# Kernel optimization log

Hardware: AMD Instinct MI355X
Metric: run time of the kernel (lower is better)

## Reference

```python
import jax, jax.numpy as jnp
import numpy as np

B, T, H, D = 1, 4096, 8, 64
CHUNK = 1024
SCALE = 0.125  # 1/sqrt(head_size)
EPS = 1e-6


def setup_inputs() -> dict:
    key = jax.random.key(0)
    k1, k2, k3, k4 = jax.random.split(key, 4)
    q = jax.random.normal(k1, (B, T, H, D), jnp.float32)
    k = jax.random.normal(k2, (B, T, H, D), jnp.float32)
    v = jax.random.normal(k3, (B, T, H, D), jnp.float32)
    # log gates: small negative values (log of per-token decay in (0,1])
    log_g = -0.05 * jax.random.uniform(k4, (B, T, H), jnp.float32)
    return {"q": q, "k": k, "v": v, "log_g": log_g}


def _power_retention(q, k, v, log_g):
    """Chunked degree-2 power retention with log-gating.

    score(t,s) = exp(g_t - g_s) * (scale * q_t . k_s)^2  (causal),
    where g = cumsum(log_g). Cross-chunk part carried via expanded state
    S[h,d,e,v] = sum_s w_s k_d k_e v  (phi(k) = k (x) k, since (q.k)^2 = phi(q).phi(k))
    and sum-of-keys normalizer s[h,d,e]. out = num / max(den, eps).
    """
    Bq, Tq, Hq, Dq = q.shape
    C, L = Tq // CHUNK, CHUNK
    qs = (q * SCALE).reshape(Bq, C, L, Hq, Dq)   # fold scale into q
    kc = k.reshape(Bq, C, L, Hq, Dq)
    vc = v.reshape(Bq, C, L, Hq, Dq)
    g = jnp.cumsum(log_g.reshape(Bq, C, L, Hq), axis=2)  # [B,C,L,H] in-chunk cum gate
    g_end = g[:, :, -1, :]                                # [B,C,H]

    # ---- intra-chunk (parallel form) ----
    scores = jnp.einsum('bclhd,bcshd->bclsh', qs, kc)          # [B,C,L,S,H]
    logdec = g[:, :, :, None, :] - g[:, :, None, :, :]          # g_t - g_s
    causal = jnp.arange(L)[:, None] >= jnp.arange(L)[None, :]
    A = jnp.where(causal[None, None, :, :, None],
                  jnp.exp(logdec) * scores * scores, 0.0)       # [B,C,L,S,H]
    intra = jnp.einsum('bclsh,bcshv->bclhv', A, vc)             # [B,C,L,H,Dv]
    row = A.sum(axis=3)                                         # [B,C,L,H]

    # ---- per-chunk state contributions ----
    wk = jnp.exp(g_end[:, :, None, :] - g)                      # key-side decay to chunk end
    kw = kc * wk[..., None]
    P = jnp.einsum('bclhd,bclhe,bclhv->bchdev', kw, kc, vc)     # [B,C,H,D,D,Dv]
    Z = jnp.einsum('bclhd,bclhe->bchde', kw, kc)                # [B,C,H,D,D]
    qdec = jnp.exp(g)                                           # query-side decay from chunk start
    gtot = jnp.exp(g_end)                                       # whole-chunk decay

    def step(carry, xs):
        S, sk = carry
        qc, Pc, Zc, gd, gt = xs   # qc [B,L,H,D], Pc [B,H,D,D,Dv], gd [B,L,H], gt [B,H]
        inter = jnp.einsum('blhd,blhe,bhdev->blhv', qc, qc, S) * gd[..., None]
        den_i = jnp.einsum('blhd,blhe,bhde->blh', qc, qc, sk) * gd
        S = gt[:, :, None, None, None] * S + Pc
        sk = gt[:, :, None, None] * sk + Zc
        return (S, sk), (inter, den_i)

    S0 = jnp.zeros((Bq, Hq, Dq, Dq, Dq), q.dtype)
    sk0 = jnp.zeros((Bq, Hq, Dq, Dq), q.dtype)
    xs = (jnp.moveaxis(qs, 1, 0), jnp.moveaxis(P, 1, 0), jnp.moveaxis(Z, 1, 0),
          jnp.moveaxis(qdec, 1, 0), jnp.moveaxis(gtot, 1, 0))
    (_, _), (inter, den_i) = jax.lax.scan(step, (S0, sk0), xs)
    inter = jnp.moveaxis(inter, 0, 1)   # [B,C,L,H,Dv]
    den_i = jnp.moveaxis(den_i, 0, 1)   # [B,C,L,H]

    num = intra + inter
    den = jnp.maximum(row + den_i, EPS)
    out = num / den[..., None]
    return out.reshape(Bq, Tq, Hq, Dq)


def reference(q, k, v, log_g):
    return _power_retention(q, k, v, log_g)
```

## Files before the change

kernel.cpp:

```cpp
#include <hip/hip_runtime.h>
#include <math.h>

typedef float f32x4 __attribute__((ext_vector_type(4)));
typedef __bf16 bf16x8 __attribute__((ext_vector_type(8)));
typedef __bf16 bf16x4 __attribute__((ext_vector_type(4)));

namespace {
constexpr int NC = 4, CL = 1024, NH = 8, ND = 64;
constexpr float KSCALE = 0.125f, KEPS = 1e-6f;
constexpr int PQ = 72;
constexpr int PK = 40;
}

#define MFMA(a,b,c) __builtin_amdgcn_mfma_f32_16x16x32_bf16((a),(b),(c),0,0,0)

__global__ __launch_bounds__(1024) void gate_kernel(const float* __restrict__ lg,
    float* __restrict__ g_arr, float* __restrict__ gend, float* __restrict__ gtot) {
  int c = blockIdx.x >> 3, h = blockIdx.x & 7;
  int l = threadIdx.x;
  __shared__ float sm[CL];
  sm[l] = lg[(c*CL + l)*NH + h];
  __syncthreads();
  for (int off = 1; off < CL; off <<= 1) {
    float t = (l >= off) ? sm[l-off] : 0.f;
    __syncthreads();
    sm[l] += t;
    __syncthreads();
  }
  g_arr[(c*NH + h)*CL + l] = sm[l];
  if (l == 0) { gend[c*NH+h] = sm[CL-1]; gtot[c*NH+h] = expf(sm[CL-1]); }
}

__global__ __launch_bounds__(256) void convert_kernel(const float* __restrict__ q,
    const float* __restrict__ k, const float* __restrict__ v,
    const float* __restrict__ g_arr, const float* __restrict__ gend,
    __bf16* __restrict__ qgb, __bf16* __restrict__ kgb,
    __bf16* __restrict__ kht, __bf16* __restrict__ vt) {
  int lt = blockIdx.x, h = blockIdx.y, c = blockIdx.z;
  int ch = c*NH + h;
  int t = threadIdx.x;
  __shared__ float ld[64][65];
  int lr = t >> 2, sg = t & 3;
  int l = lt*64 + lr;
  size_t ib = ((size_t)(c*CL + l)*NH + h)*ND + sg*16;
  float ge = gend[ch];
  float gl = g_arr[ch*CL + l];
  float eq = expf(0.5f*gl), ekk = expf(-0.5f*gl), ew = expf(0.5f*(ge-gl));
  float qv[16], kv[16], vv[16];
  #pragma unroll
  for (int i = 0; i < 4; ++i) {
    *(f32x4*)&qv[4*i] = *(const f32x4*)&q[ib+4*i];
    *(f32x4*)&kv[4*i] = *(const f32x4*)&k[ib+4*i];
    *(f32x4*)&vv[4*i] = *(const f32x4*)&v[ib+4*i];
  }
  size_t ob = ((size_t)ch*CL + l)*ND + sg*16;
  {
    bf16x8 a, b;
    #pragma unroll
    for (int i = 0; i < 8; ++i) { a[i]=(__bf16)(qv[i]*KSCALE*eq); b[i]=(__bf16)(qv[8+i]*KSCALE*eq); }
    *(bf16x8*)&qgb[ob] = a; *(bf16x8*)&qgb[ob+8] = b;
    #pragma unroll
    for (int i = 0; i < 8; ++i) { a[i]=(__bf16)(kv[i]*ekk); b[i]=(__bf16)(kv[8+i]*ekk); }
    *(bf16x8*)&kgb[ob] = a; *(bf16x8*)&kgb[ob+8] = b;
  }
  #pragma unroll
  for (int i = 0; i < 16; ++i) ld[lr][sg*16+i] = kv[i]*ew;
  __syncthreads();
  {
    int d = t >> 2, s2 = t & 3;
    bf16x8 a, b;
    #pragma unroll
    for (int i = 0; i < 8; ++i) { a[i]=(__bf16)ld[s2*16+i][d]; b[i]=(__bf16)ld[s2*16+8+i][d]; }
    size_t kb = ((size_t)ch*ND + d)*CL + lt*64 + s2*16;
    *(bf16x8*)&kht[kb] = a; *(bf16x8*)&kht[kb+8] = b;
  }
  __syncthreads();
  #pragma unroll
  for (int i = 0; i < 16; ++i) ld[lr][sg*16+i] = vv[i];
  __syncthreads();
  {
    int p = t >> 2, s2 = t & 3;
    bf16x8 a, b;
    #pragma unroll
    for (int i = 0; i < 8; ++i) { a[i]=(__bf16)ld[s2*16+i][p]; b[i]=(__bf16)ld[s2*16+8+i][p]; }
    size_t vb = ((size_t)ch*80 + p)*CL + lt*64 + s2*16;
    *(bf16x8*)&vt[vb] = a; *(bf16x8*)&vt[vb+8] = b;
  }
  if (t < 64) vt[((size_t)ch*80 + 64)*CL + lt*64 + t] = (__bf16)1.0f;
  for (int idx = t; idx < 15*64; idx += 256)
    vt[((size_t)ch*80 + 65 + idx/64)*CL + lt*64 + (idx & 63)] = (__bf16)0.0f;
}

__global__ __launch_bounds__(256) void intra_kernel(const __bf16* __restrict__ qgb,
    const __bf16* __restrict__ kgb, const __bf16* __restrict__ vt,
    float* __restrict__ out, float* __restrict__ rowp) {
  int rt = blockIdx.x, h = blockIdx.y, c = blockIdx.z;
  int ch = c*NH + h;
  int t = threadIdx.x, wv = t >> 6, lane = t & 63, qq = lane >> 4, lm = lane & 15;
  __shared__ __align__(16) __bf16 qt[64*PQ];
  __shared__ __align__(16) __bf16 kgl[32*PQ];
  __shared__ __align__(16) __bf16 vtl[80*PK];
  __shared__ __align__(16) __bf16 As[64*PK];
  {
    int r = t >> 2, sg = t & 3;
    size_t gb = ((size_t)ch*CL + rt*64 + r)*ND + sg*16;
    *(bf16x8*)&qt[r*PQ + sg*16]     = *(const bf16x8*)&qgb[gb];
    *(bf16x8*)&qt[r*PQ + sg*16 + 8] = *(const bf16x8*)&qgb[gb+8];
  }
  __syncthreads();
  bf16x8 bq0 = *(bf16x8*)&qt[(wv*16+lm)*PQ + qq*8];
  bf16x8 bq1 = *(bf16x8*)&qt[(wv*16+lm)*PQ + 32 + qq*8];
  f32x4 acc[5];
  #pragma unroll
  for (int n = 0; n < 5; ++n) acc[n] = (f32x4){0.f,0.f,0.f,0.f};
  int r_gc = rt*64 + wv*16 + lm;
  int nst = 2*rt + 2;
  for (int s3 = 0; s3 < nst; ++s3) {
    __syncthreads();
    {
      int r = t >> 3, sg = t & 7;
      *(bf16x8*)&kgl[r*PQ + sg*8] =
        *(const bf16x8*)&kgb[((size_t)ch*CL + s3*32 + r)*ND + sg*8];
      int r2 = t >> 2, s2 = t & 3;
      *(bf16x8*)&vtl[r2*PK + s2*8] =
        *(const bf16x8*)&vt[((size_t)ch*80 + r2)*CL + s3*32 + s2*8];
      if (t < 64)
        *(bf16x8*)&vtl[(64+r2)*PK + s2*8] =
          *(const bf16x8*)&vt[((size_t)ch*80 + 64 + r2)*CL + s3*32 + s2*8];
    }
    __syncthreads();
    #pragma unroll
    for (int ss = 0; ss < 2; ++ss) {
      f32x4 dr = (f32x4){0.f,0.f,0.f,0.f};
      bf16x8 a0 = *(bf16x8*)&kgl[(ss*16+lm)*PQ + qq*8];
      bf16x8 a1 = *(bf16x8*)&kgl[(ss*16+lm)*PQ + 32 + qq*8];
      dr = MFMA(a0, bq0, dr);
      dr = MFMA(a1, bq1, dr);
      bf16x4 pk;
      #pragma unroll
      for (int j = 0; j < 4; ++j) {
        int s_g = s3*32 + ss*16 + qq*4 + j;
        float dv = dr[j];
        pk[j] = (__bf16)((s_g <= r_gc) ? dv*dv : 0.f);
      }
      *(bf16x4*)&As[(wv*16+lm)*PK + ss*16 + qq*4] = pk;
    }
    bf16x8 aav = *(bf16x8*)&As[(wv*16+lm)*PK + qq*8];
    #pragma unroll
    for (int n = 0; n < 5; ++n) {
      bf16x8 bv = *(bf16x8*)&vtl[(n*16+lm)*PK + qq*8];
      acc[n] = MFMA(aav, bv, acc[n]);
    }
  }
  if (c == 0) {
    #pragma unroll
    for (int j = 0; j < 4; ++j) {
      float rs = __shfl(acc[4][j], lane & 48, 64);
      float dinv = 1.f / fmaxf(rs, KEPS);
      int rg = rt*64 + wv*16 + qq*4 + j;
      size_t ob = ((size_t)(c*CL + rg)*NH + h)*ND + lm;
      #pragma unroll
      for (int n = 0; n < 4; ++n) out[ob + 16*n] = acc[n][j]*dinv;
    }
  } else {
    #pragma unroll
    for (int j = 0; j < 4; ++j) {
      int rg = rt*64 + wv*16 + qq*4 + j;
      size_t ob = ((size_t)(c*CL + rg)*NH + h)*ND + lm;
      #pragma unroll
      for (int n = 0; n < 4; ++n) out[ob + 16*n] = acc[n][j];
      if (lm == 0) rowp[ch*CL + rg] = acc[4][j];
    }
  }
}

__global__ __launch_bounds__(256) void pzscan_kernel(const __bf16* __restrict__ kht,
    const __bf16* __restrict__ vt, const float* __restrict__ gtot,
    __bf16* __restrict__ st) {
  int mblk = blockIdx.x, h = blockIdx.y;
  int t = threadIdx.x, wv = t >> 6, lane = t & 63, qq = lane >> 4, lm = lane & 15;
  __shared__ __align__(16) __bf16 ke[64*PK];
  __shared__ __align__(16) __bf16 kd[2*PK];
  __shared__ __align__(16) __bf16 vtl[80*PK];
  __shared__ float tb[64][72];
  int dl = wv >> 1, e0w = (wv & 1)*32;
  f32x4 S_reg[2][5];
  #pragma unroll
  for (int m = 0; m < 2; ++m)
    #pragma unroll
    for (int n = 0; n < 5; ++n) S_reg[m][n] = (f32x4){0.f,0.f,0.f,0.f};
  for (int cc = 0; cc < 3; ++cc) {
    int ch = cc*NH + h;
    f32x4 acc[2][5];
    #pragma unroll
    for (int m = 0; m < 2; ++m)
      #pragma unroll
      for (int n = 0; n < 5; ++n) acc[m][n] = (f32x4){0.f,0.f,0.f,0.f};
    for (int kk = 0; kk < 32; ++kk) {
      int l0 = kk*32;
      __syncthreads();
      {
        int r = t >> 2, sg = t & 3;
        *(bf16x8*)&ke[r*PK + sg*8] =
          *(const bf16x8*)&kht[((size_t)ch*ND + r)*CL + l0 + sg*8];
        *(bf16x8*)&vtl[r*PK + sg*8] =
          *(const bf16x8*)&vt[((size_t)ch*80 + r)*CL + l0 + sg*8];
        if (t < 64)
          *(bf16x8*)&vtl[(64+r)*PK + sg*8] =
            *(const bf16x8*)&vt[((size_t)ch*80 + 64 + r)*CL + l0 + sg*8];
        if (t < 8)
          *(bf16x8*)&kd[(t>>2)*PK + (t&3)*8] =
            *(const bf16x8*)&kht[((size_t)ch*ND + mblk*2 + (t>>2))*CL + l0 + (t&3)*8];
      }
      __syncthreads();
      bf16x8 kd8 = *(bf16x8*)&kd[dl*PK + qq*8];
      bf16x8 am[2];
      #pragma unroll
      for (int m = 0; m < 2; ++m) {
        bf16x8 ke8 = *(bf16x8*)&ke[(e0w + 16*m + lm)*PK + qq*8];
        bf16x8 a;
        #pragma unroll
        for (int i = 0; i < 8; ++i) a[i] = (__bf16)((float)kd8[i] * (float)ke8[i]);
        am[m] = a;
      }
      #pragma unroll
      for (int n = 0; n < 5; ++n) {
        bf16x8 bv = *(bf16x8*)&vtl[(16*n+lm)*PK + qq*8];
        acc[0][n] = MFMA(am[0], bv, acc[0][n]);
        acc[1][n] = MFMA(am[1], bv, acc[1][n]);
      }
    }
    float gt = gtot[ch];
    #pragma unroll
    for (int m = 0; m < 2; ++m)
      #pragma unroll
      for (int n = 0; n < 5; ++n)
        #pragma unroll
        for (int j = 0; j < 4; ++j) S_reg[m][n][j] = gt*S_reg[m][n][j] + acc[m][n][j];
    size_t slab = (size_t)(cc*NH + h)*80;
    for (int h2 = 0; h2 < 2; ++h2) {
      __syncthreads();
      if (dl == h2) {
        #pragma unroll
        for (int m = 0; m < 2; ++m)
          #pragma unroll
          for (int n = 0; n < 4; ++n)
            #pragma unroll
            for (int j = 0; j < 4; ++j)
              tb[e0w + 16*m + qq*4 + j][16*n + lm] = S_reg[m][n][j];
      }
      __syncthreads();
      {
        int vr = t >> 2, es = t & 3;
        bf16x8 a, b;
        #pragma unroll
        for (int i = 0; i < 8; ++i) { a[i]=(__bf16)tb[es*16+i][vr]; b[i]=(__bf16)tb[es*16+8+i][vr]; }
        size_t sb = (slab + vr)*4096 + (size_t)(mblk*2 + h2)*64 + es*16;
        *(bf16x8*)&st[sb] = a; *(bf16x8*)&st[sb+8] = b;
      }
    }
    if (lm == 0) {
      #pragma unroll
      for (int m = 0; m < 2; ++m)
        #pragma unroll
        for (int j = 0; j < 4; ++j)
          st[(slab + 64)*4096 + (size_t)(mblk*2 + dl)*64 + e0w + 16*m + qq*4 + j] =
            (__bf16)S_reg[m][4][j];
    }
  }
}

__global__ __launch_bounds__(256) void inter_partial_kernel(
    const __bf16* __restrict__ qgb, const __bf16* __restrict__ st,
    float* __restrict__ pnum, float* __restrict__ pden) {
  int mb = blockIdx.x;
  int ks = blockIdx.y;
  int hc = blockIdx.z;
  int slab = hc >> 3, h = hc & 7;
  int c = slab + 1, ch = c*NH + h;
  int t = threadIdx.x, wv = t >> 6, lane = t & 63, qq = lane >> 4, lm = lane & 15;
  __shared__ __align__(16) __bf16 stl[2][65*PQ];
  size_t slabbase = (size_t)(slab*NH + h)*80;
  int rrow = mb*64 + wv*16 + lm;
  size_t qb = ((size_t)ch*CL + rrow)*ND;
  bf16x8 qe0 = *(const bf16x8*)&qgb[qb + qq*8];
  bf16x8 qe1 = *(const bf16x8*)&qgb[qb + 32 + qq*8];
  float qd[16];
  {
    bf16x8 qa = *(const bf16x8*)&qgb[qb + ks*16];
    bf16x8 qbv = *(const bf16x8*)&qgb[qb + ks*16 + 8];
    #pragma unroll
    for (int i = 0; i < 8; ++i) { qd[i] = (float)qa[i]; qd[8+i] = (float)qbv[i]; }
  }
  int r = t >> 2, cg = t & 3;
  bf16x8 sa, sb, sc;
  auto load_ph = [&](int ph) {
    size_t base = (slabbase + r)*4096 + (size_t)(ks*16 + ph)*64 + cg*16;
    sa = *(const bf16x8*)&st[base];
    sb = *(const bf16x8*)&st[base + 8];
    if (t < 8) sc = *(const bf16x8*)&st[(slabbase + 64)*4096 + (size_t)(ks*16 + ph)*64 + t*8];
  };
  auto write_ph = [&](int buf) {
    *(bf16x8*)&stl[buf][r*PQ + cg*16]     = sa;
    *(bf16x8*)&stl[buf][r*PQ + cg*16 + 8] = sb;
    if (t < 8) *(bf16x8*)&stl[buf][64*PQ + t*8] = sc;
  };
  f32x4 acc[5];
  #pragma unroll
  for (int n = 0; n < 5; ++n) acc[n] = (f32x4){0.f,0.f,0.f,0.f};
  load_ph(0);
  write_ph(0);
  __syncthreads();
  #pragma unroll
  for (int ph = 0; ph < 16; ++ph) {
    int buf = ph & 1;
    if (ph < 15) load_ph(ph + 1);
    float qdv = qd[ph];
    #pragma unroll
    for (int s = 0; s < 2; ++s) {
      bf16x8 qe = s ? qe1 : qe0;
      bf16x8 a;
      #pragma unroll
      for (int i = 0; i < 8; ++i) a[i] = (__bf16)(qdv * (float)qe[i]);
      #pragma unroll
      for (int n = 0; n < 5; ++n) {
        bf16x8 bv = *(bf16x8*)&stl[buf][(16*n + lm)*PQ + s*32 + qq*8];
        acc[n] = MFMA(a, bv, acc[n]);
      }
    }
    if (ph < 15) write_ph(buf ^ 1);
    __syncthreads();
  }
  size_t prow = (size_t)hc*1024 + mb*64 + wv*16;
  #pragma unroll
  for (int j = 0; j < 4; ++j) {
    int rloc = qq*4 + j;
    #pragma unroll
    for (int n = 0; n < 4; ++n)
      atomicAdd(&pnum[(prow + rloc)*64 + 16*n + lm], acc[n][j]);
    if (lm == 0) atomicAdd(&pden[prow + rloc], acc[4][j]);
  }
}

__global__ __launch_bounds__(256) void finalize_kernel(const float* __restrict__ rowp,
    const float* __restrict__ pnum, const float* __restrict__ pden,
    float* __restrict__ out) {
  int idx = blockIdx.x*256 + threadIdx.x;
  int e4 = idx*4;
  int row = e4 >> 6;
  int col = e4 & 63;
  int hc = row >> 10, rg = row & 1023;
  int slab = hc >> 3, h = hc & 7, c = slab + 1;
  float dinv = 1.f / fmaxf(rowp[(c*NH + h)*CL + rg] + pden[row], KEPS);
  f32x4 pv = *(const f32x4*)&pnum[e4];
  size_t ob = ((size_t)(c*CL + rg)*NH + h)*ND + col;
  f32x4 ov = *(const f32x4*)&out[ob];
  #pragma unroll
  for (int j = 0; j < 4; ++j) ov[j] = (ov[j] + pv[j]) * dinv;
  *(f32x4*)&out[ob] = ov;
}

extern "C" void kernel_launch(void* const* d_in, const int* in_sizes, int n_in,
                              void* d_out, int out_size, void* d_ws, size_t ws_size,
                              hipStream_t stream) {
  const float* q  = (const float*)d_in[0];
  const float* k  = (const float*)d_in[1];
  const float* v  = (const float*)d_in[2];
  const float* lg = (const float*)d_in[3];
  float* out = (float*)d_out;

  float* wf    = (float*)d_ws;
  float* g_arr = wf;
  float* gend  = g_arr + 32768;
  float* gtot  = gend + 32;
  float* rowp  = gtot + 32;
  float* pden  = rowp + 32768;
  float* pnum  = pden + 24576;
  __bf16* qgb  = (__bf16*)(pnum + 1572864);
  __bf16* kgb  = qgb + 2097152;
  __bf16* kht  = kgb + 2097152;
  __bf16* vt   = kht + 2097152;
  __bf16* st   = vt + 2621440;

  hipMemsetAsync(pden, 0, (size_t)(24576 + 1572864)*sizeof(float), stream);
  gate_kernel<<<dim3(NC*NH), dim3(CL), 0, stream>>>(lg, g_arr, gend, gtot);
  convert_kernel<<<dim3(16, NH, NC), dim3(256), 0, stream>>>(q, k, v, g_arr, gend, qgb, kgb, kht, vt);
  intra_kernel<<<dim3(16, NH, NC), dim3(256), 0, stream>>>(qgb, kgb, vt, out, rowp);
  pzscan_kernel<<<dim3(32, NH), dim3(256), 0, stream>>>(kht, vt, gtot, st);
  inter_partial_kernel<<<dim3(16, 4, 24), dim3(256), 0, stream>>>(qgb, st, pnum, pden);
  finalize_kernel<<<dim3(1536), dim3(256), 0, stream>>>(rowp, pnum, pden, out);
}
```

Baseline: 243.7 us.

## Double-buffer shared-memory tiles with register prefetch in intra and pzscan kernels

Converts the intra and pzscan kernels' LDS tile loads into a register-prefetch, double-buffered pipeline. The next tile's global loads are issued before the current tile's MFMA work, and the results are written to the alternate buffer afterward. This removes one of the two barriers per iteration. pzscan's three nested chunk loops are flattened into one 96-iteration loop so the prefetch spans chunk boundaries. The cost is extra LDS and registers, which may lower occupancy.

```diff
diff --git a/kernel.cpp b/kernel.cpp
--- a/kernel.cpp
+++ b/kernel.cpp
@@ -98,15 +98,31 @@
   int ch = c*NH + h;
   int t = threadIdx.x, wv = t >> 6, lane = t & 63, qq = lane >> 4, lm = lane & 15;
   __shared__ __align__(16) __bf16 qt[64*PQ];
-  __shared__ __align__(16) __bf16 kgl[32*PQ];
-  __shared__ __align__(16) __bf16 vtl[80*PK];
+  __shared__ __align__(16) __bf16 kgl[2][32*PQ];
+  __shared__ __align__(16) __bf16 vtl[2][80*PK];
   __shared__ __align__(16) __bf16 As[64*PK];
+  int nst = 2*rt + 2;
+  int r8 = t >> 3, sg8 = t & 7;
+  int r4 = t >> 2, s4 = t & 3;
+  bf16x8 rkg, rva, rvb;
+  auto load_it = [&](int s3) {
+    rkg = *(const bf16x8*)&kgb[((size_t)ch*CL + s3*32 + r8)*ND + sg8*8];
+    rva = *(const bf16x8*)&vt[((size_t)ch*80 + r4)*CL + s3*32 + s4*8];
+    if (t < 64) rvb = *(const bf16x8*)&vt[((size_t)ch*80 + 64 + r4)*CL + s3*32 + s4*8];
+  };
+  auto write_it = [&](int buf) {
+    *(bf16x8*)&kgl[buf][r8*PQ + sg8*8] = rkg;
+    *(bf16x8*)&vtl[buf][r4*PK + s4*8] = rva;
+    if (t < 64) *(bf16x8*)&vtl[buf][(64+r4)*PK + s4*8] = rvb;
+  };
   {
     int r = t >> 2, sg = t & 3;
     size_t gb = ((size_t)ch*CL + rt*64 + r)*ND + sg*16;
     *(bf16x8*)&qt[r*PQ + sg*16]     = *(const bf16x8*)&qgb[gb];
     *(bf16x8*)&qt[r*PQ + sg*16 + 8] = *(const bf16x8*)&qgb[gb+8];
   }
+  load_it(0);
+  write_it(0);
   __syncthreads();
   bf16x8 bq0 = *(bf16x8*)&qt[(wv*16+lm)*PQ + qq*8];
   bf16x8 bq1 = *(bf16x8*)&qt[(wv*16+lm)*PQ + 32 + qq*8];
@@ -114,26 +130,14 @@
   #pragma unroll
   for (int n = 0; n < 5; ++n) acc[n] = (f32x4){0.f,0.f,0.f,0.f};
   int r_gc = rt*64 + wv*16 + lm;
-  int nst = 2*rt + 2;
+  int buf = 0;
   for (int s3 = 0; s3 < nst; ++s3) {
-    __syncthreads();
-    {
-      int r = t >> 3, sg = t & 7;
-      *(bf16x8*)&kgl[r*PQ + sg*8] =
-        *(const bf16x8*)&kgb[((size_t)ch*CL + s3*32 + r)*ND + sg*8];
-      int r2 = t >> 2, s2 = t & 3;
-      *(bf16x8*)&vtl[r2*PK + s2*8] =
-        *(const bf16x8*)&vt[((size_t)ch*80 + r2)*CL + s3*32 + s2*8];
-      if (t < 64)
-        *(bf16x8*)&vtl[(64+r2)*PK + s2*8] =
-          *(const bf16x8*)&vt[((size_t)ch*80 + 64 + r2)*CL + s3*32 + s2*8];
-    }
-    __syncthreads();
+    if (s3 + 1 < nst) load_it(s3 + 1);
     #pragma unroll
     for (int ss = 0; ss < 2; ++ss) {
       f32x4 dr = (f32x4){0.f,0.f,0.f,0.f};
-      bf16x8 a0 = *(bf16x8*)&kgl[(ss*16+lm)*PQ + qq*8];
-      bf16x8 a1 = *(bf16x8*)&kgl[(ss*16+lm)*PQ + 32 + qq*8];
+      bf16x8 a0 = *(bf16x8*)&kgl[buf][(ss*16+lm)*PQ + qq*8];
+      bf16x8 a1 = *(bf16x8*)&kgl[buf][(ss*16+lm)*PQ + 32 + qq*8];
       dr = MFMA(a0, bq0, dr);
       dr = MFMA(a1, bq1, dr);
       bf16x4 pk;
@@ -148,9 +152,12 @@
     bf16x8 aav = *(bf16x8*)&As[(wv*16+lm)*PK + qq*8];
     #pragma unroll
     for (int n = 0; n < 5; ++n) {
-      bf16x8 bv = *(bf16x8*)&vtl[(n*16+lm)*PK + qq*8];
+      bf16x8 bv = *(bf16x8*)&vtl[buf][(n*16+lm)*PK + qq*8];
       acc[n] = MFMA(aav, bv, acc[n]);
     }
+    if (s3 + 1 < nst) write_it(buf ^ 1);
+    __syncthreads();
+    buf ^= 1;
   }
   if (c == 0) {
     #pragma unroll
@@ -179,93 +186,103 @@
     __bf16* __restrict__ st) {
   int mblk = blockIdx.x, h = blockIdx.y;
   int t = threadIdx.x, wv = t >> 6, lane = t & 63, qq = lane >> 4, lm = lane & 15;
-  __shared__ __align__(16) __bf16 ke[64*PK];
-  __shared__ __align__(16) __bf16 kd[2*PK];
-  __shared__ __align__(16) __bf16 vtl[80*PK];
+  __shared__ __align__(16) __bf16 ke[2][64*PK];
+  __shared__ __align__(16) __bf16 kd[2][2*PK];
+  __shared__ __align__(16) __bf16 vtl[2][80*PK];
   __shared__ float tb[64][72];
   int dl = wv >> 1, e0w = (wv & 1)*32;
-  f32x4 S_reg[2][5];
+  int r = t >> 2, cg = t & 3;
+  bf16x8 rke, rva, rvb, rkd;
+  auto load_it = [&](int it) {
+    int cc = it >> 5, kk = it & 31;
+    int ch = cc*NH + h;
+    int l0 = kk*32;
+    rke = *(const bf16x8*)&kht[((size_t)ch*ND + r)*CL + l0 + cg*8];
+    rva = *(const bf16x8*)&vt[((size_t)ch*80 + r)*CL + l0 + cg*8];
+    if (t < 64) rvb = *(const bf16x8*)&vt[((size_t)ch*80 + 64 + r)*CL + l0 + cg*8];
+    if (t < 8)  rkd = *(const bf16x8*)&kht[((size_t)ch*ND + mblk*2 + (t>>2))*CL + l0 + (t&3)*8];
+  };
+  auto write_it = [&](int buf) {
+    *(bf16x8*)&ke[buf][r*PK + cg*8] = rke;
+    *(bf16x8*)&vtl[buf][r*PK + cg*8] = rva;
+    if (t < 64) *(bf16x8*)&vtl[buf][(64+r)*PK + cg*8] = rvb;
+    if (t < 8)  *(bf16x8*)&kd[buf][(t>>2)*PK + (t&3)*8] = rkd;
+  };
+  f32x4 S_reg[2][5], acc[2][5];
   #pragma unroll
   for (int m = 0; m < 2; ++m)
     #pragma unroll
-    for (int n = 0; n < 5; ++n) S_reg[m][n] = (f32x4){0.f,0.f,0.f,0.f};
-  for (int cc = 0; cc < 3; ++cc) {
-    int ch = cc*NH + h;
-    f32x4 acc[2][5];
-    #pragma unroll
-    for (int m = 0; m < 2; ++m)
-      #pragma unroll
-      for (int n = 0; n < 5; ++n) acc[m][n] = (f32x4){0.f,0.f,0.f,0.f};
-    for (int kk = 0; kk < 32; ++kk) {
-      int l0 = kk*32;
-      __syncthreads();
-      {
-        int r = t >> 2, sg = t & 3;
-        *(bf16x8*)&ke[r*PK + sg*8] =
-          *(const bf16x8*)&kht[((size_t)ch*ND + r)*CL + l0 + sg*8];
-        *(bf16x8*)&vtl[r*PK + sg*8] =
-          *(const bf16x8*)&vt[((size_t)ch*80 + r)*CL + l0 + sg*8];
-        if (t < 64)
-          *(bf16x8*)&vtl[(64+r)*PK + sg*8] =
-            *(const bf16x8*)&vt[((size_t)ch*80 + 64 + r)*CL + l0 + sg*8];
-        if (t < 8)
-          *(bf16x8*)&kd[(t>>2)*PK + (t&3)*8] =
-            *(const bf16x8*)&kht[((size_t)ch*ND + mblk*2 + (t>>2))*CL + l0 + (t&3)*8];
+    for (int n = 0; n < 5; ++n) {
+      S_reg[m][n] = (f32x4){0.f,0.f,0.f,0.f};
+      acc[m][n] = (f32x4){0.f,0.f,0.f,0.f};
+    }
+  load_it(0);
+  write_it(0);
+  __syncthreads();
+  int buf = 0;
+  for (int it = 0; it < 96; ++it) {
+    if (it < 95) load_it(it + 1);
+    bf16x8 kd8 = *(bf16x8*)&kd[buf][dl*PK + qq*8];
+    bf16x8 am[2];
+    #pragma unroll
+    for (int m = 0; m < 2; ++m) {
+      bf16x8 ke8 = *(bf16x8*)&ke[buf][(e0w + 16*m + lm)*PK + qq*8];
+      bf16x8 a;
+      #pragma unroll
+      for (int i = 0; i < 8; ++i) a[i] = (__bf16)((float)kd8[i] * (float)ke8[i]);
+      am[m] = a;
+    }
+    #pragma unroll
+    for (int n = 0; n < 5; ++n) {
+      bf16x8 bv = *(bf16x8*)&vtl[buf][(16*n+lm)*PK + qq*8];
+      acc[0][n] = MFMA(am[0], bv, acc[0][n]);
+      acc[1][n] = MFMA(am[1], bv, acc[1][n]);
+    }
+    if (it < 95) write_it(buf ^ 1);
+    __syncthreads();
+    buf ^= 1;
+    if ((it & 31) == 31) {
+      int cc = it >> 5;
+      float gt = gtot[cc*NH + h];
+      #pragma unroll
+      for (int m = 0; m < 2; ++m)
+        #pragma unroll
+        for (int n = 0; n < 5; ++n)
+          #pragma unroll
+          for (int j = 0; j < 4; ++j) {
+            S_reg[m][n][j] = gt*S_reg[m][n][j] + acc[m][n][j];
+            acc[m][n][j] = 0.f;
+          }
+      size_t slab = (size_t)(cc*NH + h)*80;
+      for (int h2 = 0; h2 < 2; ++h2) {
+        __syncthreads();
+        if (dl == h2) {
+          #pragma unroll
+          for (int m = 0; m < 2; ++m)
+            #pragma unroll
+            for (int n = 0; n < 4; ++n)
+              #pragma unroll
+              for (int j = 0; j < 4; ++j)
+                tb[e0w + 16*m + qq*4 + j][16*n + lm] = S_reg[m][n][j];
+        }
+        __syncthreads();
+        {
+          int vr = t >> 2, es = t & 3;
+          bf16x8 a, b;
+          #pragma unroll
+          for (int i = 0; i < 8; ++i) { a[i]=(__bf16)tb[es*16+i][vr]; b[i]=(__bf16)tb[es*16+8+i][vr]; }
+          size_t sb = (slab + vr)*4096 + (size_t)(mblk*2 + h2)*64 + es*16;
+          *(bf16x8*)&st[sb] = a; *(bf16x8*)&st[sb+8] = b;
+        }
       }
-      __syncthreads();
-      bf16x8 kd8 = *(bf16x8*)&kd[dl*PK + qq*8];
-      bf16x8 am[2];
-      #pragma unroll
-      for (int m = 0; m < 2; ++m) {
-        bf16x8 ke8 = *(bf16x8*)&ke[(e0w + 16*m + lm)*PK + qq*8];
-        bf16x8 a;
-        #pragma unroll
-        for (int i = 0; i < 8; ++i) a[i] = (__bf16)((float)kd8[i] * (float)ke8[i]);
-        am[m] = a;
-      }
-      #pragma unroll
-      for (int n = 0; n < 5; ++n) {
-        bf16x8 bv = *(bf16x8*)&vtl[(16*n+lm)*PK + qq*8];
-        acc[0][n] = MFMA(am[0], bv, acc[0][n]);
-        acc[1][n] = MFMA(am[1], bv, acc[1][n]);
-      }
-    }
-    float gt = gtot[ch];
-    #pragma unroll
-    for (int m = 0; m < 2; ++m)
-      #pragma unroll
-      for (int n = 0; n < 5; ++n)
-        #pragma unroll
-        for (int j = 0; j < 4; ++j) S_reg[m][n][j] = gt*S_reg[m][n][j] + acc[m][n][j];
-    size_t slab = (size_t)(cc*NH + h)*80;
-    for (int h2 = 0; h2 < 2; ++h2) {
-      __syncthreads();
-      if (dl == h2) {
+      if (lm == 0) {
         #pragma unroll
         for (int m = 0; m < 2; ++m)
           #pragma unroll
-          for (int n = 0; n < 4; ++n)
-            #pragma unroll
-            for (int j = 0; j < 4; ++j)
-              tb[e0w + 16*m + qq*4 + j][16*n + lm] = S_reg[m][n][j];
+          for (int j = 0; j < 4; ++j)
+            st[(slab + 64)*4096 + (size_t)(mblk*2 + dl)*64 + e0w + 16*m + qq*4 + j] =
+              (__bf16)S_reg[m][4][j];
       }
-      __syncthreads();
-      {
-        int vr = t >> 2, es = t & 3;
-        bf16x8 a, b;
-        #pragma unroll
-        for (int i = 0; i < 8; ++i) { a[i]=(__bf16)tb[es*16+i][vr]; b[i]=(__bf16)tb[es*16+8+i][vr]; }
-        size_t sb = (slab + vr)*4096 + (size_t)(mblk*2 + h2)*64 + es*16;
-        *(bf16x8*)&st[sb] = a; *(bf16x8*)&st[sb+8] = b;
-      }
-    }
-    if (lm == 0) {
-      #pragma unroll
-      for (int m = 0; m < 2; ++m)
-        #pragma unroll
-        for (int j = 0; j < 4; ++j)
-          st[(slab + 64)*4096 + (size_t)(mblk*2 + dl)*64 + e0w + 16*m + qq*4 + j] =
-            (__bf16)S_reg[m][4][j];
     }
   }
 }
```

Result: faster. 215.6 us (-11.5%).
